# Performance work log

Measured on AMD Instinct MI355X. Metric: run time of the kernel, lower is better.

Reference implementation:

```python
import jax, jax.numpy as jnp
import numpy as np

MAXDISP = 128  # from init_kwargs; 3*MAXDISP == 384 == enc0 in_planes

# 24 census offsets in a 5x5 window (center (2,2) skipped), order as in torch source
OFFSETS = [(0,0),(1,0),(2,0),(3,0),(4,0),(0,1),(1,1),(2,1),(3,1),(4,1),
           (0,2),(1,2),(3,2),(4,2),(0,3),(1,3),(2,3),(3,3),(4,3),
           (0,4),(1,4),(2,4),(3,4),(4,4)]


def rgb_to_ycbcr(img):
    # img: (n,3,h,w)
    r, g, b = img[:, 0], img[:, 1], img[:, 2]
    y = 0.299 * r + 0.587 * g + 0.114 * b
    cb = (b - y) * 0.564 + 0.5
    cr = (r - y) * 0.713 + 0.5
    return jnp.stack([y, cb, cr], axis=1)


def avg_pool2(x):
    n, c, h, w = x.shape
    return x.reshape(n, c, h // 2, 2, w // 2, 2).mean(axis=(3, 5))


def census5(img):
    # img: (n,1,h,w) float -> (n,1,h,w) int32, 24-bit census code, 2px zero border
    n, c, h, w = img.shape
    center = img[:, :, 2:h - 2, 2:w - 2]
    # (24, n, 1, h-4, w-4) boolean comparisons, exactly the torch offset order
    bits = jnp.stack([(img[:, :, v:v + h - 4, u:u + w - 4] >= center)
                      for (u, v) in OFFSETS], axis=0).astype(jnp.int32)
    weights = (2 ** jnp.arange(23, -1, -1)).astype(jnp.int32)  # census = census*2 + bit fold
    cen = jnp.tensordot(weights, bits, axes=1)
    return jnp.pad(cen, ((0, 0), (0, 0), (2, 2), (2, 2)))


def cost_volume(l, r, maxdisp, op):
    # l, r: (n,1,h,w). out[:, d, :, x] = op(l[x+d], r[x]) for x < w-d else 0,
    # matching torch's slice (left[d:w] vs right[0:w-d]) + right-pad with zeros.
    w = l.shape[-1]
    xs = jnp.arange(w)

    def per_d(d):
        l_sh = jnp.roll(l, -d, axis=-1)          # l_sh[..., x] = l[..., x+d] (wrapped part masked)
        c = op(l_sh, r)
        return jnp.where(xs < w - d, c, jnp.zeros_like(c))

    cv = jax.vmap(per_d)(jnp.arange(maxdisp))    # (D, n, 1, h, w)
    return cv[:, :, 0].transpose(1, 0, 2, 3)     # (n, D, h, w)


def setup_inputs() -> dict:
    key = jax.random.key(0)
    k1, k2 = jax.random.split(key)
    left = jax.random.uniform(k1, (2, 3, 384, 1280), dtype=jnp.float32)
    right = jax.random.uniform(k2, (2, 3, 384, 1280), dtype=jnp.float32)
    return {"left": left, "right": right}


def reference(left, right):
    # FDSCS front-end: half-res YCbCr, census+Hamming on Y, abs-diff on Cb/Cr, unify
    lp, rp = avg_pool2(left), avg_pool2(right)
    lyuv, ryuv = rgb_to_ycbcr(lp), rgb_to_ycbcr(rp)

    lc = census5(lyuv[:, 0:1])
    rc = census5(ryuv[:, 0:1])
    # Hamming distance = popcount of 24-bit XOR (codes < 2^24, so popcount == 24-bit loop)
    ham = cost_volume(lc, rc, MAXDISP,
                      lambda a, b: jax.lax.population_count(jnp.bitwise_xor(a, b))
                      ).astype(jnp.float32)
    u = cost_volume(lyuv[:, 1:2], ryuv[:, 1:2], MAXDISP, lambda a, b: jnp.abs(a - b))
    v = cost_volume(lyuv[:, 2:3], ryuv[:, 2:3], MAXDISP, lambda a, b: jnp.abs(a - b))

    # Unify_size normalization constants from torch source
    y_n = (ham - 11.08282948) / 0.1949711
    u_n = (u - 0.02175535) / 35.91432953
    v_n = (v - 0.02679042) / 26.79782867
    return jnp.concatenate([y_n, u_n, v_n], axis=1)  # (n, 3*MAXDISP, h/2, w/2)
```

## Files before the change

kernel.cpp:

```cpp
#include <hip/hip_runtime.h>

#define H   384
#define W   1280
#define PH  192
#define PW  640
#define PP  (PH*PW)

typedef float f32x4 __attribute__((ext_vector_type(4)));
typedef int   i32x4 __attribute__((ext_vector_type(4)));

__global__ __launch_bounds__(256) void pool_ycbcr_kernel(
    const float* __restrict__ left, const float* __restrict__ right,
    float* __restrict__ yp, float* __restrict__ cbp, float* __restrict__ crp)
{
    int tid = blockIdx.x * blockDim.x + threadIdx.x;
    if (tid >= 4 * PP) return;
    int p   = tid / PP;
    int rem = tid - p * PP;
    int y   = rem / PW;
    int x   = rem - y * PW;

    const float* src = (p < 2 ? left : right) + (size_t)(p & 1) * 3 * H * W;

    float pc[3];
#pragma unroll
    for (int c = 0; c < 3; ++c) {
        const float* ch = src + (size_t)c * H * W + (size_t)(2 * y) * W + 2 * x;
        float2 a = *(const float2*)ch;
        float2 b = *(const float2*)(ch + W);
        float s = __fadd_rn(__fadd_rn(__fadd_rn(a.x, a.y), b.x), b.y);
        pc[c] = __fmul_rn(s, 0.25f);
    }
    float yv = __fadd_rn(__fadd_rn(__fmul_rn(0.299f, pc[0]),
                                   __fmul_rn(0.587f, pc[1])),
                         __fmul_rn(0.114f, pc[2]));
    float cb = __fadd_rn(__fmul_rn(__fsub_rn(pc[2], yv), 0.564f), 0.5f);
    float cr = __fadd_rn(__fmul_rn(__fsub_rn(pc[0], yv), 0.713f), 0.5f);

    yp[tid]  = yv;
    cbp[tid] = cb;
    crp[tid] = cr;
}

__global__ __launch_bounds__(256) void census_kernel(
    const float* __restrict__ yp, int* __restrict__ cen)
{
    int tid = blockIdx.x * blockDim.x + threadIdx.x;
    if (tid >= 4 * PP) return;
    int p   = tid / PP;
    int rem = tid - p * PP;
    int y   = rem / PW;
    int x   = rem - y * PW;

    int code = 0;
    if (y >= 2 && y < PH - 2 && x >= 2 && x < PW - 2) {
        const float* base = yp + (size_t)p * PP;
        float c = base[y * PW + x];
        int bit = 23;
#pragma unroll
        for (int v = 0; v < 5; ++v) {
#pragma unroll
            for (int u = 0; u < 5; ++u) {
                if (u == 2 && v == 2) continue;
                float nb = base[(y - 2 + v) * PW + (x - 2 + u)];
                code |= (nb >= c ? 1 : 0) << bit;
                --bit;
            }
        }
    }
    cen[tid] = code;
}

__global__ __launch_bounds__(256) void costvol_kernel(
    const float* __restrict__ cbp, const float* __restrict__ crp,
    const int* __restrict__ cen, float* __restrict__ out)
{
    const float m1 = 11.08282948f, i1 = 1.0f / 0.1949711f;
    const float m2 = 0.02175535f,  i2 = 1.0f / 35.91432953f;
    const float m3 = 0.02679042f,  i3 = 1.0f / 26.79782867f;

    int b   = blockIdx.x;
    int n   = b / 1152;
    int r   = b - n * 1152;
    int g   = r / 384;
    int r2  = r - g * 384;
    int row = r2 >> 1;
    int dh  = r2 & 1;

    __shared__ int Ls[776];
    __shared__ int Rs[640];

    const int* Lplane;
    const int* Rplane;
    if (g == 0)      { Lplane = cen + (size_t)n * PP;
                       Rplane = cen + (size_t)(2 + n) * PP; }
    else if (g == 1) { Lplane = (const int*)(cbp + (size_t)n * PP);
                       Rplane = (const int*)(cbp + (size_t)(2 + n) * PP); }
    else             { Lplane = (const int*)(crp + (size_t)n * PP);
                       Rplane = (const int*)(crp + (size_t)(2 + n) * PP); }

    const i32x4* Lg4 = (const i32x4*)(Lplane + row * PW);
    const i32x4* Rg4 = (const i32x4*)(Rplane + row * PW);

    const int t = threadIdx.x;
    for (int j = t; j < 320; j += 256) {
        if (j < 160) *(i32x4*)&Ls[j * 4]         = Lg4[j];
        else         *(i32x4*)&Rs[(j - 160) * 4] = Rg4[j - 160];
    }
    __syncthreads();

    float* outb = out + ((size_t)(n * 384 + g * 128 + dh * 64) * PH + row) * PW;

    if (g == 0) {
        const float c0 = (0.0f - m1) * i1;
#pragma unroll 4
        for (int idx = t; idx < 64 * 160; idx += 256) {
            int dd = idx / 160;
            int q  = idx - dd * 160;
            int x0 = q * 4;
            int d  = dh * 64 + dd;
            int nvalid = PW - d;
            i32x4 rv = *(const i32x4*)&Rs[x0];
            int base = x0 + d;
            int e0 = Ls[base], e1 = Ls[base + 1], e2 = Ls[base + 2], e3 = Ls[base + 3];
            f32x4 ov;
            ov.x = (x0 + 0 < nvalid) ? ((float)__popc(e0 ^ rv.x) - m1) * i1 : c0;
            ov.y = (x0 + 1 < nvalid) ? ((float)__popc(e1 ^ rv.y) - m1) * i1 : c0;
            ov.z = (x0 + 2 < nvalid) ? ((float)__popc(e2 ^ rv.z) - m1) * i1 : c0;
            ov.w = (x0 + 3 < nvalid) ? ((float)__popc(e3 ^ rv.w) - m1) * i1 : c0;
            *(f32x4*)(outb + (size_t)dd * PP + x0) = ov;
        }
    } else {
        const float m  = (g == 1) ? m2 : m3;
        const float iv = (g == 1) ? i2 : i3;
        const float c0 = (0.0f - m) * iv;
        const float* Lf = (const float*)Ls;
        const float* Rf = (const float*)Rs;
#pragma unroll 4
        for (int idx = t; idx < 64 * 160; idx += 256) {
            int dd = idx / 160;
            int q  = idx - dd * 160;
            int x0 = q * 4;
            int d  = dh * 64 + dd;
            int nvalid = PW - d;
            f32x4 rv = *(const f32x4*)&Rf[x0];
            int base = x0 + d;
            float e0 = Lf[base], e1 = Lf[base + 1], e2 = Lf[base + 2], e3 = Lf[base + 3];
            f32x4 ov;
            ov.x = (x0 + 0 < nvalid) ? (fabsf(e0 - rv.x) - m) * iv : c0;
            ov.y = (x0 + 1 < nvalid) ? (fabsf(e1 - rv.y) - m) * iv : c0;
            ov.z = (x0 + 2 < nvalid) ? (fabsf(e2 - rv.z) - m) * iv : c0;
            ov.w = (x0 + 3 < nvalid) ? (fabsf(e3 - rv.w) - m) * iv : c0;
            *(f32x4*)(outb + (size_t)dd * PP + x0) = ov;
        }
    }
}

extern "C" void kernel_launch(void* const* d_in, const int* in_sizes, int n_in,
                              void* d_out, int out_size, void* d_ws, size_t ws_size,
                              hipStream_t stream)
{
    const float* left  = (const float*)d_in[0];
    const float* right = (const float*)d_in[1];

    float* ws  = (float*)d_ws;
    float* yp  = ws;
    float* cbp = ws + 4 * PP;
    float* crp = ws + 8 * PP;
    int*   cen = (int*)(ws + 12 * PP);

    int threads = 256;
    int blocksAB = (4 * PP + threads - 1) / threads;

    pool_ycbcr_kernel<<<blocksAB, threads, 0, stream>>>(left, right, yp, cbp, crp);
    census_kernel<<<blocksAB, threads, 0, stream>>>(yp, cen);

    int blocksC = 2 * 3 * 192 * 2;
    costvol_kernel<<<blocksC, threads, 0, stream>>>(cbp, crp, cen, (float*)d_out);
}
```

Measured before the change: 87.57 us.

## Tile cost volume by two rows and 32 disparities with padded LDS

Each costvol block now handles two adjacent image rows and a quarter of the disparities (32) instead of one row and half the disparities, with the left row stored in LDS using a one-word pad every 32 entries. The padding is meant to reduce bank conflicts on the unaligned shifted reads, and the row pairing changes the output write pattern so consecutive threads cover two rows per disparity. The total block count is unchanged. The loop now has a fixed trip count of 40, and each load pays extra index arithmetic for the padding.

```diff
diff --git a/kernel.cpp b/kernel.cpp
--- a/kernel.cpp
+++ b/kernel.cpp
@@ -5,6 +5,7 @@
 #define PH  192
 #define PW  640
 #define PP  (PH*PW)
+#define LSW 792
 
 typedef float f32x4 __attribute__((ext_vector_type(4)));
 typedef int   i32x4 __attribute__((ext_vector_type(4)));
@@ -84,11 +85,13 @@
     int r   = b - n * 1152;
     int g   = r / 384;
     int r2  = r - g * 384;
-    int row = r2 >> 1;
-    int dh  = r2 & 1;
-
-    __shared__ int Ls[776];
-    __shared__ int Rs[640];
+    int rp  = r2 >> 2;
+    int dq  = r2 & 3;
+    int row0 = rp * 2;
+    int d0   = dq * 32;
+
+    __shared__ int Ls[2][LSW];
+    __shared__ int Rs[2][640];
 
     const int* Lplane;
     const int* Rplane;
@@ -99,59 +102,78 @@
     else             { Lplane = (const int*)(crp + (size_t)n * PP);
                        Rplane = (const int*)(crp + (size_t)(2 + n) * PP); }
 
-    const i32x4* Lg4 = (const i32x4*)(Lplane + row * PW);
-    const i32x4* Rg4 = (const i32x4*)(Rplane + row * PW);
-
     const int t = threadIdx.x;
-    for (int j = t; j < 320; j += 256) {
-        if (j < 160) *(i32x4*)&Ls[j * 4]         = Lg4[j];
-        else         *(i32x4*)&Rs[(j - 160) * 4] = Rg4[j - 160];
+    for (int j = t; j < 640; j += 256) {
+        if (j < 320) {
+            int rr = j / 160;
+            int jj = j - rr * 160;
+            int o  = jj * 4;
+            *(i32x4*)&Ls[rr][o + (o >> 5)] =
+                *(const i32x4*)(Lplane + (row0 + rr) * PW + o);
+        } else {
+            int j2 = j - 320;
+            int rr = j2 / 160;
+            int jj = j2 - rr * 160;
+            *(i32x4*)&Rs[rr][jj * 4] =
+                *(const i32x4*)(Rplane + (row0 + rr) * PW + jj * 4);
+        }
     }
     __syncthreads();
 
-    float* outb = out + ((size_t)(n * 384 + g * 128 + dh * 64) * PH + row) * PW;
+    float* outb = out + ((size_t)(n * 384 + g * 128 + d0) * PH + row0) * PW;
 
     if (g == 0) {
         const float c0 = (0.0f - m1) * i1;
 #pragma unroll 4
-        for (int idx = t; idx < 64 * 160; idx += 256) {
-            int dd = idx / 160;
-            int q  = idx - dd * 160;
-            int x0 = q * 4;
-            int d  = dh * 64 + dd;
+        for (int k = 0; k < 40; ++k) {
+            int idx  = t + 256 * k;
+            int rest = idx / 160;
+            int q    = idx - rest * 160;
+            int ri   = rest & 1;
+            int dd   = rest >> 1;
+            int x0   = q * 4;
+            int d    = d0 + dd;
             int nvalid = PW - d;
-            i32x4 rv = *(const i32x4*)&Rs[x0];
-            int base = x0 + d;
-            int e0 = Ls[base], e1 = Ls[base + 1], e2 = Ls[base + 2], e3 = Ls[base + 3];
+            i32x4 rv = *(const i32x4*)&Rs[ri][x0];
+            int i0 = x0 + d, i1_ = i0 + 1, i2_ = i0 + 2, i3_ = i0 + 3;
+            int e0 = Ls[ri][i0  + (i0  >> 5)];
+            int e1 = Ls[ri][i1_ + (i1_ >> 5)];
+            int e2 = Ls[ri][i2_ + (i2_ >> 5)];
+            int e3 = Ls[ri][i3_ + (i3_ >> 5)];
             f32x4 ov;
             ov.x = (x0 + 0 < nvalid) ? ((float)__popc(e0 ^ rv.x) - m1) * i1 : c0;
             ov.y = (x0 + 1 < nvalid) ? ((float)__popc(e1 ^ rv.y) - m1) * i1 : c0;
             ov.z = (x0 + 2 < nvalid) ? ((float)__popc(e2 ^ rv.z) - m1) * i1 : c0;
             ov.w = (x0 + 3 < nvalid) ? ((float)__popc(e3 ^ rv.w) - m1) * i1 : c0;
-            *(f32x4*)(outb + (size_t)dd * PP + x0) = ov;
+            *(f32x4*)(outb + ((size_t)dd * PH + ri) * PW + x0) = ov;
         }
     } else {
         const float m  = (g == 1) ? m2 : m3;
         const float iv = (g == 1) ? i2 : i3;
         const float c0 = (0.0f - m) * iv;
-        const float* Lf = (const float*)Ls;
-        const float* Rf = (const float*)Rs;
 #pragma unroll 4
-        for (int idx = t; idx < 64 * 160; idx += 256) {
-            int dd = idx / 160;
-            int q  = idx - dd * 160;
-            int x0 = q * 4;
-            int d  = dh * 64 + dd;
+        for (int k = 0; k < 40; ++k) {
+            int idx  = t + 256 * k;
+            int rest = idx / 160;
+            int q    = idx - rest * 160;
+            int ri   = rest & 1;
+            int dd   = rest >> 1;
+            int x0   = q * 4;
+            int d    = d0 + dd;
             int nvalid = PW - d;
-            f32x4 rv = *(const f32x4*)&Rf[x0];
-            int base = x0 + d;
-            float e0 = Lf[base], e1 = Lf[base + 1], e2 = Lf[base + 2], e3 = Lf[base + 3];
+            f32x4 rv = *(const f32x4*)&Rs[ri][x0];
+            int i0 = x0 + d, i1_ = i0 + 1, i2_ = i0 + 2, i3_ = i0 + 3;
+            const float* Lf = (const float*)Ls[ri];
+            float e0 = Lf[i0  + (i0  >> 5)];
+            float e1 = Lf[i1_ + (i1_ >> 5)];
+            float e2 = Lf[i2_ + (i2_ >> 5)];
+            float e3 = Lf[i3_ + (i3_ >> 5)];
             f32x4 ov;
             ov.x = (x0 + 0 < nvalid) ? (fabsf(e0 - rv.x) - m) * iv : c0;
             ov.y = (x0 + 1 < nvalid) ? (fabsf(e1 - rv.y) - m) * iv : c0;
             ov.z = (x0 + 2 < nvalid) ? (fabsf(e2 - rv.z) - m) * iv : c0;
             ov.w = (x0 + 3 < nvalid) ? (fabsf(e3 - rv.w) - m) * iv : c0;
-            *(f32x4*)(outb + (size_t)dd * PP + x0) = ov;
+            *(f32x4*)(outb + ((size_t)dd * PH + ri) * PW + x0) = ov;
         }
     }
 }
@@ -175,6 +197,6 @@
     pool_ycbcr_kernel<<<blocksAB, threads, 0, stream>>>(left, right, yp, cbp, crp);
     census_kernel<<<blocksAB, threads, 0, stream>>>(yp, cen);
 
-    int blocksC = 2 * 3 * 192 * 2;
+    int blocksC = 2 * 3 * 96 * 4;
     costvol_kernel<<<blocksC, threads, 0, stream>>>(cbp, crp, cen, (float*)d_out);
 }
```

Measured after the change: 91.34 us. 4.3% more time.

## Fuse pooling/YCbCr and census into one tiled kernel with shared-memory halo

Applied to the files above, without the earlier changes.

Merges the pool+YCbCr kernel and the census kernel into a single kernel. Each block computes a 64x4 tile of Y plus a 2-pixel halo in shared memory, then forms census codes from it. This removes the Y-plane round trip through global memory and one kernel launch. In exchange, halo pixels are recomputed, which adds some redundant input loads, and fp contraction is disabled explicitly to keep the original rounding.

```diff
diff --git a/kernel.cpp b/kernel.cpp
--- a/kernel.cpp
+++ b/kernel.cpp
@@ -9,66 +9,71 @@
 typedef float f32x4 __attribute__((ext_vector_type(4)));
 typedef int   i32x4 __attribute__((ext_vector_type(4)));
 
-__global__ __launch_bounds__(256) void pool_ycbcr_kernel(
+__global__ __launch_bounds__(256) void fused_pre_kernel(
     const float* __restrict__ left, const float* __restrict__ right,
-    float* __restrict__ yp, float* __restrict__ cbp, float* __restrict__ crp)
+    float* __restrict__ cbp, float* __restrict__ crp, int* __restrict__ cen)
 {
-    int tid = blockIdx.x * blockDim.x + threadIdx.x;
-    if (tid >= 4 * PP) return;
-    int p   = tid / PP;
-    int rem = tid - p * PP;
-    int y   = rem / PW;
-    int x   = rem - y * PW;
+#pragma clang fp contract(off)
+    int blk = blockIdx.x;
+    int p   = blk / 480;
+    int r   = blk - p * 480;
+    int by  = r / 10;
+    int bx  = r - by * 10;
+    int X0  = bx * 64, Y0 = by * 4;
+
+    __shared__ float Ys[8][69];
 
     const float* src = (p < 2 ? left : right) + (size_t)(p & 1) * 3 * H * W;
+    const int t = threadIdx.x;
 
-    float pc[3];
+    for (int j = t; j < 544; j += 256) {
+        int hy = j / 68;
+        int hx = j - hy * 68;
+        int gx = X0 - 2 + hx;
+        int gy = Y0 - 2 + hy;
+        int cx = min(max(gx, 0), PW - 1);
+        int cy = min(max(gy, 0), PH - 1);
+
+        float pc[3];
 #pragma unroll
-    for (int c = 0; c < 3; ++c) {
-        const float* ch = src + (size_t)c * H * W + (size_t)(2 * y) * W + 2 * x;
-        float2 a = *(const float2*)ch;
-        float2 b = *(const float2*)(ch + W);
-        float s = __fadd_rn(__fadd_rn(__fadd_rn(a.x, a.y), b.x), b.y);
-        pc[c] = __fmul_rn(s, 0.25f);
+        for (int c = 0; c < 3; ++c) {
+            const float* chp = src + (size_t)c * H * W + (size_t)(2 * cy) * W + 2 * cx;
+            float2 a = *(const float2*)chp;
+            float2 b = *(const float2*)(chp + W);
+            float s = ((a.x + a.y) + b.x) + b.y;
+            pc[c] = s * 0.25f;
+        }
+        float yv = (0.299f * pc[0] + 0.587f * pc[1]) + 0.114f * pc[2];
+        Ys[hy][hx] = yv;
+
+        if (hx >= 2 && hx < 66 && hy >= 2 && hy < 6) {
+            float cb = (pc[2] - yv) * 0.564f + 0.5f;
+            float cr = (pc[0] - yv) * 0.713f + 0.5f;
+            size_t o = (size_t)p * PP + (size_t)gy * PW + gx;
+            cbp[o] = cb;
+            crp[o] = cr;
+        }
     }
-    float yv = __fadd_rn(__fadd_rn(__fmul_rn(0.299f, pc[0]),
-                                   __fmul_rn(0.587f, pc[1])),
-                         __fmul_rn(0.114f, pc[2]));
-    float cb = __fadd_rn(__fmul_rn(__fsub_rn(pc[2], yv), 0.564f), 0.5f);
-    float cr = __fadd_rn(__fmul_rn(__fsub_rn(pc[0], yv), 0.713f), 0.5f);
+    __syncthreads();
 
-    yp[tid]  = yv;
-    cbp[tid] = cb;
-    crp[tid] = cr;
-}
-
-__global__ __launch_bounds__(256) void census_kernel(
-    const float* __restrict__ yp, int* __restrict__ cen)
-{
-    int tid = blockIdx.x * blockDim.x + threadIdx.x;
-    if (tid >= 4 * PP) return;
-    int p   = tid / PP;
-    int rem = tid - p * PP;
-    int y   = rem / PW;
-    int x   = rem - y * PW;
-
+    int tx = t & 63, ty = t >> 6;
+    int gx = X0 + tx, gy = Y0 + ty;
     int code = 0;
-    if (y >= 2 && y < PH - 2 && x >= 2 && x < PW - 2) {
-        const float* base = yp + (size_t)p * PP;
-        float c = base[y * PW + x];
+    if (gx >= 2 && gx < PW - 2 && gy >= 2 && gy < PH - 2) {
+        float c = Ys[ty + 2][tx + 2];
         int bit = 23;
 #pragma unroll
         for (int v = 0; v < 5; ++v) {
 #pragma unroll
             for (int u = 0; u < 5; ++u) {
                 if (u == 2 && v == 2) continue;
-                float nb = base[(y - 2 + v) * PW + (x - 2 + u)];
+                float nb = Ys[ty + v][tx + u];
                 code |= (nb >= c ? 1 : 0) << bit;
                 --bit;
             }
         }
     }
-    cen[tid] = code;
+    cen[(size_t)p * PP + (size_t)gy * PW + gx] = code;
 }
 
 __global__ __launch_bounds__(256) void costvol_kernel(
@@ -164,17 +169,13 @@
     const float* right = (const float*)d_in[1];
 
     float* ws  = (float*)d_ws;
-    float* yp  = ws;
-    float* cbp = ws + 4 * PP;
-    float* crp = ws + 8 * PP;
-    int*   cen = (int*)(ws + 12 * PP);
+    float* cbp = ws;
+    float* crp = ws + 4 * PP;
+    int*   cen = (int*)(ws + 8 * PP);
 
-    int threads = 256;
-    int blocksAB = (4 * PP + threads - 1) / threads;
-
-    pool_ycbcr_kernel<<<blocksAB, threads, 0, stream>>>(left, right, yp, cbp, crp);
-    census_kernel<<<blocksAB, threads, 0, stream>>>(yp, cen);
+    int blocksPre = 4 * 48 * 10;
+    fused_pre_kernel<<<blocksPre, 256, 0, stream>>>(left, right, cbp, crp, cen);
 
     int blocksC = 2 * 3 * 192 * 2;
-    costvol_kernel<<<blocksC, threads, 0, stream>>>(cbp, crp, cen, (float*)d_out);
+    costvol_kernel<<<blocksC, 256, 0, stream>>>(cbp, crp, cen, (float*)d_out);
 }
```

After: 88.36 us. About the same (+0.9%).
